# Performance work log

Hardware: AMD Instinct MI355X
Metric: run time of the kernel (lower is better)

## Reference

```python
import jax, jax.numpy as jnp
import numpy as np
import math

V, BS, D, L, H = 50257, 1024, 768, 12, 4
DH = D // H  # 192
B, T = 4, 1024


def setup_inputs() -> dict:
    key = jax.random.key(0)
    ks = jax.random.split(key, 18)
    s = 0.02
    inp = {
        "x": jax.random.randint(ks[0], (B, T), 0, V),
        "tok_emb": jax.random.normal(ks[1], (V, D), jnp.float32) * s,
        "pos_emb": jax.random.normal(ks[2], (BS, D), jnp.float32) * s,
        "ln1_s": jnp.ones((L, D), jnp.float32),
        "ln1_b": jnp.zeros((L, D), jnp.float32),
        "qkv_w": jax.random.normal(ks[3], (L, D, 3 * D), jnp.float32) * s,
        "qkv_b": jnp.zeros((L, 3 * D), jnp.float32),
        "ln2_s": jnp.ones((L, D), jnp.float32),
        "ln2_b": jnp.zeros((L, D), jnp.float32),
        "fc_w": jax.random.normal(ks[4], (L, D, 4 * D), jnp.float32) * s,
        "fc_b": jnp.zeros((L, 4 * D), jnp.float32),
        "proj_w": jax.random.normal(ks[5], (L, 4 * D, D), jnp.float32) * s,
        "proj_b": jnp.zeros((L, D), jnp.float32),
        "lnf_s": jnp.ones((D,), jnp.float32),
        "lnf_b": jnp.zeros((D,), jnp.float32),
        "head_w": jax.random.normal(ks[6], (D, V), jnp.float32) * s,
        "head_b": jnp.zeros((V,), jnp.float32),
    }
    return inp


def _ln(x, scale, shift):
    m = x.mean(-1, keepdims=True)
    v = jnp.mean((x - m) ** 2, axis=-1, keepdims=True)
    return (x - m) * jax.lax.rsqrt(v + 1e-5) * scale + shift


def _forward(x, tok_emb, pos_emb, ln1_s, ln1_b, qkv_w, qkv_b, ln2_s, ln2_b,
             fc_w, fc_b, proj_w, proj_b, lnf_s, lnf_b, head_w, head_b):
    Bx, Tx = x.shape
    h = tok_emb[x] + pos_emb[:Tx]  # [B,T,D]
    causal = jnp.tril(jnp.ones((Tx, Tx), bool))
    scale = 1.0 / math.sqrt(DH)

    def block(h, p):
        s1, b1, wq, bq, s2, b2, wf, bf, wp, bp = p
        # attention (no output projection, faithful to source)
        ln1 = _ln(h, s1, b1)
        qkv = ln1 @ wq + bq  # [B,T,3D]
        q, k, v = jnp.split(qkv, 3, axis=-1)
        q = q.reshape(Bx, Tx, H, DH)
        k = k.reshape(Bx, Tx, H, DH)
        v = v.reshape(Bx, Tx, H, DH)
        att = jnp.einsum('bthd,bshd->bhts', q, k) * scale
        att = jnp.where(causal, att, -jnp.inf)
        att = jax.nn.softmax(att, axis=-1)
        y = jnp.einsum('bhts,bshd->bthd', att, v).reshape(Bx, Tx, D)
        h = h + y
        # MLP (ReLU, despite attr named gelu in source)
        ln2 = _ln(h, s2, b2)
        m = jax.nn.relu(ln2 @ wf + bf) @ wp + bp
        return h + m, None

    h, _ = jax.lax.scan(block, h,
                        (ln1_s, ln1_b, qkv_w, qkv_b, ln2_s, ln2_b,
                         fc_w, fc_b, proj_w, proj_b))
    h = _ln(h, lnf_s, lnf_b)
    return h @ head_w + head_b  # [B,T,V]


def reference(x, tok_emb, pos_emb, ln1_s, ln1_b, qkv_w, qkv_b, ln2_s, ln2_b,
              fc_w, fc_b, proj_w, proj_b, lnf_s, lnf_b, head_w, head_b):
    return _forward(x, tok_emb, pos_emb, ln1_s, ln1_b, qkv_w, qkv_b,
                    ln2_s, ln2_b, fc_w, fc_b, proj_w, proj_b,
                    lnf_s, lnf_b, head_w, head_b)
```

## Files before the change

kernel.cpp:

```cpp
#include <hip/hip_runtime.h>
#include <stdint.h>

#define D_MODEL 768
#define NHEAD 4
#define DHEAD 192
#define SEQ 1024
#define NLAYER 12
#define NTOK 4096
#define NVOCAB 50257

typedef __attribute__((ext_vector_type(4))) float f32x4;
typedef __attribute__((ext_vector_type(4))) int i32x4;
typedef __attribute__((ext_vector_type(4))) unsigned short u16x4;

__device__ __forceinline__ unsigned short f2bf(float f) {
  unsigned u = __builtin_bit_cast(unsigned, f);
  u += 0x7FFFu + ((u >> 16) & 1u);
  return (unsigned short)(u >> 16);
}

#define GLDS(src, dst)                                                   \
  __builtin_amdgcn_global_load_lds(                                      \
      (const __attribute__((address_space(1))) void*)(src),              \
      (__attribute__((address_space(3))) void*)(dst), 16, 0, 0)

#define FENCE asm volatile("" ::: "memory")
#define BAR()                         \
  do {                                \
    FENCE;                            \
    __builtin_amdgcn_s_barrier();     \
    FENCE;                            \
  } while (0)

__global__ __launch_bounds__(256) void embed_kernel(
    const int* __restrict__ x, const float* __restrict__ tok,
    const float* __restrict__ pos, float* __restrict__ h) {
  int row = blockIdx.x;
  int t = row & (SEQ - 1);
  int id = x[row];
  const float* tp = tok + (long)id * D_MODEL;
  const float* pp = pos + (long)t * D_MODEL;
  float* hp = h + (long)row * D_MODEL;
  for (int j = threadIdx.x; j < D_MODEL; j += 256)
    hp[j] = tp[j] + pp[j];
}

__global__ __launch_bounds__(256) void ln_kernel(
    const float* __restrict__ h, const float* __restrict__ sc,
    const float* __restrict__ sh, unsigned short* __restrict__ out) {
  __shared__ float red[4];
  int row = blockIdx.x;
  const float* x = h + (long)row * D_MODEL;
  int tid = threadIdx.x;
  float v0 = x[tid], v1 = x[tid + 256], v2 = x[tid + 512];
  float s = v0 + v1 + v2;
  for (int o = 32; o > 0; o >>= 1) s += __shfl_xor(s, o);
  if ((tid & 63) == 0) red[tid >> 6] = s;
  __syncthreads();
  float mean = (red[0] + red[1] + red[2] + red[3]) * (1.0f / D_MODEL);
  __syncthreads();
  float d0 = v0 - mean, d1 = v1 - mean, d2 = v2 - mean;
  float q = d0 * d0 + d1 * d1 + d2 * d2;
  for (int o = 32; o > 0; o >>= 1) q += __shfl_xor(q, o);
  if ((tid & 63) == 0) red[tid >> 6] = q;
  __syncthreads();
  float var = (red[0] + red[1] + red[2] + red[3]) * (1.0f / D_MODEL);
  float r = rsqrtf(var + 1e-5f);
  unsigned short* op = out + (long)row * D_MODEL;
  op[tid]       = f2bf(d0 * r * sc[tid]       + sh[tid]);
  op[tid + 256] = f2bf(d1 * r * sc[tid + 256] + sh[tid + 256]);
  op[tid + 512] = f2bf(d2 * r * sc[tid + 512] + sh[tid + 512]);
}

__global__ __launch_bounds__(256) void wtrans3_kernel(
    const float* __restrict__ qw, const float* __restrict__ fw,
    const float* __restrict__ pw, unsigned short* __restrict__ tq,
    unsigned short* __restrict__ tf, unsigned short* __restrict__ tp) {
  __shared__ unsigned short tile[32][33];
  int bid = blockIdx.x;
  const float* src; unsigned short* dst; int K, N, nb;
  if (bid < 1728)               { src = qw; dst = tq; K = 768;  N = 2304; nb = 72; }
  else if ((bid -= 1728) < 2304){ src = fw; dst = tf; K = 768;  N = 3072; nb = 96; }
  else { bid -= 2304;             src = pw; dst = tp; K = 3072; N = 768;  nb = 24; }
  int n0 = (bid % nb) * 32, k0 = (bid / nb) * 32;
  int tx = threadIdx.x & 31, ty = threadIdx.x >> 5;
  #pragma unroll
  for (int i = 0; i < 4; ++i) {
    int k = k0 + ty + i * 8;
    tile[ty + i * 8][tx] = f2bf(src[(long)k * N + n0 + tx]);
  }
  __syncthreads();
  #pragma unroll
  for (int i = 0; i < 4; ++i) {
    int nn = n0 + ty + i * 8;
    dst[(long)nn * K + k0 + tx] = tile[tx][ty + i * 8];
  }
}

__global__ __launch_bounds__(256) void wtrans_kernel(
    const float* __restrict__ w, unsigned short* __restrict__ wt, int K, int N) {
  __shared__ unsigned short tile[32][33];
  int n0 = blockIdx.x * 32, k0 = blockIdx.y * 32;
  int tx = threadIdx.x, ty = threadIdx.y;
  int n = n0 + tx; if (n >= N) n = N - 1;
  #pragma unroll
  for (int i = 0; i < 4; ++i) {
    int k = k0 + ty + i * 8;
    tile[ty + i * 8][tx] = f2bf(w[(long)k * N + n]);
  }
  __syncthreads();
  #pragma unroll
  for (int i = 0; i < 4; ++i) {
    int nn = n0 + ty + i * 8;
    if (nn < N) wt[(long)nn * K + k0 + tx] = tile[tx][ty + i * 8];
  }
}

__global__ __launch_bounds__(256) void vt_kernel(
    const unsigned short* __restrict__ qkv, unsigned short* __restrict__ vt) {
  __shared__ unsigned short tile[32][33];
  int bh = blockIdx.z, b = bh >> 2, hh = bh & 3;
  int t0 = blockIdx.x * 32, f0 = blockIdx.y * 32;
  int tx = threadIdx.x, ty = threadIdx.y;
  const unsigned short* src = qkv + (long)b * SEQ * 2304 + 2 * D_MODEL + hh * DHEAD;
  #pragma unroll
  for (int i = 0; i < 4; ++i) {
    int t = t0 + ty + i * 8;
    tile[ty + i * 8][tx] = src[(long)t * 2304 + f0 + tx];
  }
  __syncthreads();
  unsigned short* dst = vt + (long)bh * DHEAD * SEQ;
  #pragma unroll
  for (int i = 0; i < 4; ++i) {
    int f = f0 + ty + i * 8;
    dst[(long)f * SEQ + t0 + tx] = tile[tx][ty + i * 8];
  }
}

__global__ __launch_bounds__(256) void fattn2_kernel(
    const unsigned short* __restrict__ qkv,
    const unsigned short* __restrict__ vt,
    float* __restrict__ h) {
  __shared__ float slds[16][1024];
  __shared__ unsigned short plds[16][1024];
  const float rscale = 0.07216878364870323f;
  int tid = threadIdx.x;
  int lane = tid & 63, wid = tid >> 6;
  int l15 = lane & 15, g = lane >> 4;
  int bid = blockIdx.x;
  int bh = bid & 15;
  int p = bid >> 4;
  int qt = (p < 32) ? (63 - p) : (p - 32);
  int b = bh >> 2, hh = bh & 3;
  const unsigned short* Qb = qkv + ((long)b * 1024 + qt * 16) * 2304 + hh * 192;
  const unsigned short* Kb = qkv + (long)b * 1024 * 2304 + 768 + hh * 192;
  const unsigned short* Vb = vt + (long)bh * 192 * 1024;
  int smax = qt * 16 + 16;
  int smax32 = (smax + 31) & ~31;

  i32x4 qfr[6];
  #pragma unroll
  for (int kb = 0; kb < 6; ++kb)
    qfr[kb] = *(const i32x4*)(Qb + (long)l15 * 2304 + kb * 32 + g * 8);
  int nsf = smax >> 4;
  int sfw = (nsf + 3) >> 2;
  int sf0 = wid * sfw;
  int sf1 = min(sf0 + sfw, nsf);
  for (int sf = sf0; sf < sf1; ++sf) {
    f32x4 sacc = {};
    #pragma unroll
    for (int kb = 0; kb < 6; ++kb) {
      i32x4 kf = *(const i32x4*)(Kb + (long)(sf * 16 + l15) * 2304 + kb * 32 + g * 8);
      asm("v_mfma_f32_16x16x32_bf16 %0, %1, %2, %0"
          : "+v"(sacc) : "v"(kf), "v"(qfr[kb]));
    }
    asm volatile("s_nop 7\n\ts_nop 7\n\ts_nop 7" : "+v"(sacc));
    f32x4 st;
    #pragma unroll
    for (int e = 0; e < 4; ++e) st[e] = sacc[e] * rscale;
    *(f32x4*)&slds[l15][sf * 16 + 4 * g] = st;
  }
  __syncthreads();

  {
    int q = tid >> 4, lane16 = tid & 15;
    int qg = qt * 16 + q;
    float mx = -3.0e38f;
    for (int s = lane16 * 4; s < smax32; s += 64) {
      f32x4 v = *(const f32x4*)&slds[q][s];
      #pragma unroll
      for (int e = 0; e < 4; ++e)
        if (s + e <= qg) mx = fmaxf(mx, v[e]);
    }
    #pragma unroll
    for (int o = 1; o < 16; o <<= 1) mx = fmaxf(mx, __shfl_xor(mx, o));
    float sum = 0.f;
    for (int s = lane16 * 4; s < smax32; s += 64) {
      f32x4 v = *(const f32x4*)&slds[q][s];
      #pragma unroll
      for (int e = 0; e < 4; ++e)
        v[e] = (s + e <= qg) ? __expf(v[e] - mx) : 0.f;
      *(f32x4*)&slds[q][s] = v;
      sum += v[0] + v[1] + v[2] + v[3];
    }
    #pragma unroll
    for (int o = 1; o < 16; o <<= 1) sum += __shfl_xor(sum, o);
    float inv = 1.0f / sum;
    for (int s = lane16 * 4; s < smax32; s += 64) {
      f32x4 v = *(const f32x4*)&slds[q][s];
      u16x4 o;
      #pragma unroll
      for (int e = 0; e < 4; ++e) o[e] = f2bf(v[e] * inv);
      *(u16x4*)&plds[q][s] = o;
    }
  }
  __syncthreads();

  f32x4 acc[3] = {};
  for (int ss = 0; ss < smax32; ss += 32) {
    i32x4 pf = *(const i32x4*)&plds[l15][ss + g * 8];
    #pragma unroll
    for (int nf = 0; nf < 3; ++nf) {
      i32x4 vf = *(const i32x4*)(Vb + (long)(wid * 48 + nf * 16 + l15) * 1024 + ss + g * 8);
      asm("v_mfma_f32_16x16x32_bf16 %0, %1, %2, %0"
          : "+v"(acc[nf]) : "v"(vf), "v"(pf));
    }
  }
  asm volatile("s_nop 7\n\ts_nop 7\n\ts_nop 7"
               : "+v"(acc[0]), "+v"(acc[1]), "+v"(acc[2]));
  float* hp = h + ((long)b * 1024 + qt * 16 + l15) * 768 + hh * 192 + wid * 48;
  #pragma unroll
  for (int nf = 0; nf < 3; ++nf) {
    float* cp = hp + nf * 16 + 4 * g;
    f32x4 old = *(f32x4*)cp;
    #pragma unroll
    for (int e = 0; e < 4; ++e) old[e] += acc[nf][e];
    *(f32x4*)cp = old;
  }
}

template<int MODE>
__global__ __launch_bounds__(512, 2) void gemm256_kernel(
    const unsigned short* __restrict__ A,
    const unsigned short* __restrict__ B,
    const float* __restrict__ bias,
    void* __restrict__ Cv, int ldc,
    int M, int N, int K, int mb) {
  __shared__ __align__(16) unsigned short lds[2][2][2][128 * 64];

  int tid = threadIdx.x;
  int lane = tid & 63;
  int wid = tid >> 6;
  int wm = wid >> 2;
  int wn = wid & 3;

  int bid = blockIdx.x;
  int mpx = mb >> 3;
  int xcd = bid & 7;
  int c = bid >> 3;
  int m0 = (xcd * mpx + (c & (mpx - 1))) * 256;
  int n0 = (c / mpx) * 256;

  auto stageA = [&](int buf, int half, int kt) {
    const unsigned short* src = A + (long)(m0 + half * 128) * K + kt * 64;
    #pragma unroll
    for (int i = 0; i < 2; ++i) {
      int chunk = i * 8 + wid;
      int r = chunk * 8 + (lane >> 3);
      int cc = ((lane & 7) ^ (lane >> 3)) << 3;
      GLDS(src + (long)r * K + cc, &lds[buf][0][half][chunk * 512]);
    }
  };
  auto stageB = [&](int buf, int half, int kt) {
    #pragma unroll
    for (int i = 0; i < 2; ++i) {
      int chunk = i * 8 + wid;
      int r = chunk * 8 + (lane >> 3);
      int cc = ((lane & 7) ^ (lane >> 3)) << 3;
      int rg = n0 + half * 128 + r;
      if (rg >= N) rg = N - 1;
      GLDS(B + (long)rg * K + kt * 64 + cc, &lds[buf][1][half][chunk * 512]);
    }
  };

  auto lda_frag = [&](int buf, int f, int s) -> i32x4 {
    int r = wm * 64 + (f & 3) * 16 + (lane & 15);
    int kb = s * 64 + ((lane >> 4) << 4);
    int off = r * 128 + (kb ^ ((r & 7) << 4));
    return *(const i32x4*)((const char*)&lds[buf][0][f >> 2][0] + off);
  };
  auto ldb_frag = [&](int buf, int gg, int s) -> i32x4 {
    int r = wn * 32 + (gg & 1) * 16 + (lane & 15);
    int kb = s * 64 + ((lane >> 4) << 4);
    int off = r * 128 + (kb ^ ((r & 7) << 4));
    return *(const i32x4*)((const char*)&lds[buf][1][gg >> 1][0] + off);
  };

  f32x4 acc[8][4] = {};
  i32x4 a[4][2], b[4][2];

  int nt = K / 64;

  stageA(0, 0, 0); stageB(0, 0, 0); stageB(0, 1, 0); stageA(0, 1, 0);
  stageA(1, 0, 1); stageB(1, 0, 1); stageB(1, 1, 1);
  asm volatile("s_waitcnt vmcnt(6)" ::: "memory");
  BAR();

  for (int t = 0; t < nt; ++t) {
    int buf = t & 1, nbuf = buf ^ 1;
    #pragma unroll
    for (int fi = 0; fi < 4; ++fi) {
      a[fi][0] = lda_frag(buf, fi, 0);
      a[fi][1] = lda_frag(buf, fi, 1);
    }
    #pragma unroll
    for (int gi = 0; gi < 2; ++gi) {
      b[gi][0] = ldb_frag(buf, gi, 0);
      b[gi][1] = ldb_frag(buf, gi, 1);
    }
    if (t + 1 < nt) stageA(nbuf, 1, t + 1);
    BAR();
    __builtin_amdgcn_s_setprio(1);
    #pragma unroll
    for (int s = 0; s < 2; ++s)
      #pragma unroll
      for (int fi = 0; fi < 4; ++fi)
        #pragma unroll
        for (int gi = 0; gi < 2; ++gi)
          asm("v_mfma_f32_16x16x32_bf16 %0, %1, %2, %0"
              : "+v"(acc[fi][gi]) : "v"(b[gi][s]), "v"(a[fi][s]));
    __builtin_amdgcn_s_setprio(0);
    BAR();
    #pragma unroll
    for (int gi = 2; gi < 4; ++gi) {
      b[gi][0] = ldb_frag(buf, gi, 0);
      b[gi][1] = ldb_frag(buf, gi, 1);
    }
    if (t + 2 < nt) stageA(buf, 0, t + 2);
    BAR();
    __builtin_amdgcn_s_setprio(1);
    #pragma unroll
    for (int s = 0; s < 2; ++s)
      #pragma unroll
      for (int fi = 0; fi < 4; ++fi)
        #pragma unroll
        for (int gi = 2; gi < 4; ++gi)
          asm("v_mfma_f32_16x16x32_bf16 %0, %1, %2, %0"
              : "+v"(acc[fi][gi]) : "v"(b[gi][s]), "v"(a[fi][s]));
    __builtin_amdgcn_s_setprio(0);
    BAR();
    #pragma unroll
    for (int fi = 0; fi < 4; ++fi) {
      a[fi][0] = lda_frag(buf, 4 + fi, 0);
      a[fi][1] = lda_frag(buf, 4 + fi, 1);
    }
    if (t + 2 < nt) stageB(buf, 0, t + 2);
    BAR();
    __builtin_amdgcn_s_setprio(1);
    #pragma unroll
    for (int s = 0; s < 2; ++s)
      #pragma unroll
      for (int fi = 0; fi < 4; ++fi)
        #pragma unroll
        for (int gi = 2; gi < 4; ++gi)
          asm("v_mfma_f32_16x16x32_bf16 %0, %1, %2, %0"
              : "+v"(acc[4 + fi][gi]) : "v"(b[gi][s]), "v"(a[fi][s]));
    __builtin_amdgcn_s_setprio(0);
    BAR();
    if (t + 2 < nt) {
      stageB(buf, 1, t + 2);
      asm volatile("s_waitcnt vmcnt(6)" ::: "memory");
    } else if (t + 1 < nt) {
      asm volatile("s_waitcnt vmcnt(0)" ::: "memory");
    }
    BAR();
    __builtin_amdgcn_s_setprio(1);
    #pragma unroll
    for (int s = 0; s < 2; ++s)
      #pragma unroll
      for (int fi = 0; fi < 4; ++fi)
        #pragma unroll
        for (int gi = 0; gi < 2; ++gi)
          asm("v_mfma_f32_16x16x32_bf16 %0, %1, %2, %0"
              : "+v"(acc[4 + fi][gi]) : "v"(b[gi][s]), "v"(a[fi][s]));
    __builtin_amdgcn_s_setprio(0);
    BAR();
  }

  int cr = lane & 15;
  int cg = (lane >> 4) << 2;
  #pragma unroll
  for (int f = 0; f < 8; ++f) {
    long row = m0 + wm * 64 + (f & 3) * 16 + (f >> 2) * 128 + cr;
    #pragma unroll
    for (int gg = 0; gg < 4; ++gg) {
      int col = n0 + wn * 32 + (gg & 1) * 16 + (gg >> 1) * 128 + cg;
      f32x4 v = acc[f][gg];
      if (MODE == 0 || MODE == 1) {
        f32x4 bv = *(const f32x4*)(bias + col);
        u16x4 o;
        #pragma unroll
        for (int r = 0; r < 4; ++r) {
          float tt = v[r] + bv[r];
          if (MODE == 1) tt = fmaxf(tt, 0.f);
          o[r] = f2bf(tt);
        }
        *(u16x4*)((unsigned short*)Cv + row * (long)ldc + col) = o;
      } else {
        float* cp = (float*)Cv + row * (long)ldc + col;
        if (col + 4 <= N) {
          f32x4 bv = *(const f32x4*)(bias + col);
          f32x4 o;
          #pragma unroll
          for (int r = 0; r < 4; ++r) o[r] = v[r] + bv[r];
          *(f32x4*)cp = o;
        } else {
          #pragma unroll
          for (int r = 0; r < 4; ++r)
            if (col + r < N) cp[r] = v[r] + bias[col + r];
        }
      }
    }
  }
}

#define BM 128
#define BN 128
#define BKK 32

template<int MODE>
__global__ __launch_bounds__(256) void gemm_kernel(
    const unsigned short* __restrict__ A, int lda,
    const unsigned short* __restrict__ B, int ldb,
    const float* __restrict__ bias,
    void* __restrict__ Cv, int ldc,
    int M, int N, int K,
    int NI, long sAo, long sAi, long sBo, long sBi,
    long sCo, long sCi, float alpha, int causal, int mblocks) {
  __shared__ __align__(16) unsigned short As[2][BM * BKK];
  __shared__ __align__(16) unsigned short Bs[2][BN * BKK];
  int z = blockIdx.z;
  int zo = z / NI, zi = z - zo * NI;
  A += zo * sAo + zi * sAi;
  B += zo * sBo + zi * sBi;
  long coff = zo * sCo + zi * sCi;

  int m0, n0;
  if (mblocks > 0) {
    int bid = blockIdx.x;
    int mpx = mblocks >> 3;
    int xcd = bid & 7;
    int c = bid >> 3;
    m0 = (xcd * mpx + (c & (mpx - 1))) * BM;
    n0 = (c / mpx) * BN;
  } else {
    m0 = blockIdx.y * BM;
    n0 = blockIdx.x * BN;
  }
  if (causal == 1 && n0 > m0 + BM - 1) return;
  int kmax = (causal == 2) ? min(K, m0 + BM) : K;

  int tid = threadIdx.x;
  int lane = tid & 63;
  int wave = tid >> 6;
  int wm = (wave >> 1) * 64;
  int wn = (wave & 1) * 64;

  auto stage = [&](int buf, int k0) {
    #pragma unroll
    for (int i = 0; i < 2; ++i) {
      int c0 = i * 256 + wave * 64;
      int cc = c0 + lane;
      int row = cc >> 2;
      int ko = (cc & 3) << 3;
      GLDS(A + (long)(m0 + row) * lda + k0 + ko, As[buf] + c0 * 8);
      int rg = n0 + row; if (rg >= N) rg = N - 1;
      GLDS(B + (long)rg * ldb + k0 + ko, Bs[buf] + c0 * 8);
    }
  };

  f32x4 acc[4][4] = {};
  int nt = kmax / BKK;
  stage(0, 0);
  __syncthreads();
  int cur = 0;
  for (int t = 0; t < nt; ++t) {
    if (t + 1 < nt) stage(cur ^ 1, (t + 1) * BKK);
    int lr = lane & 15;
    int kg = (lane >> 4) << 3;
    i32x4 af[4], bf[4];
    #pragma unroll
    for (int mi = 0; mi < 4; ++mi)
      af[mi] = *(const i32x4*)(As[cur] + (wm + mi * 16 + lr) * BKK + kg);
    #pragma unroll
    for (int ni = 0; ni < 4; ++ni)
      bf[ni] = *(const i32x4*)(Bs[cur] + (wn + ni * 16 + lr) * BKK + kg);
    #pragma unroll
    for (int mi = 0; mi < 4; ++mi)
      #pragma unroll
      for (int ni = 0; ni < 4; ++ni)
        asm("v_mfma_f32_16x16x32_bf16 %0, %1, %2, %0"
            : "+v"(acc[mi][ni]) : "v"(bf[ni]), "v"(af[mi]));
    __syncthreads();
    cur ^= 1;
  }

  int cm = lane & 15;
  int cg = (lane >> 4) << 2;
  #pragma unroll
  for (int mi = 0; mi < 4; ++mi) {
    long row = m0 + wm + mi * 16 + cm;
    #pragma unroll
    for (int ni = 0; ni < 4; ++ni) {
      int col = n0 + wn + ni * 16 + cg;
      f32x4 v = acc[mi][ni];
      if (MODE == 2) {
        #pragma unroll
        for (int r = 0; r < 4; ++r) v[r] *= alpha;
        *(f32x4*)((float*)Cv + coff + row * (long)ldc + col) = v;
      } else if (MODE == 0 || MODE == 1) {
        f32x4 bv = *(const f32x4*)(bias + col);
        u16x4 o;
        #pragma unroll
        for (int r = 0; r < 4; ++r) {
          float t = v[r] + bv[r];
          if (MODE == 1) t = fmaxf(t, 0.f);
          o[r] = f2bf(t);
        }
        *(u16x4*)((unsigned short*)Cv + coff + row * (long)ldc + col) = o;
      } else {
        float* cp = (float*)Cv + coff + row * (long)ldc + col;
        if (col + 4 <= N) {
          f32x4 bv = bias ? *(const f32x4*)(bias + col)
                          : f32x4{0.f, 0.f, 0.f, 0.f};
          if (MODE == 3) {
            f32x4 old = *(f32x4*)cp;
            #pragma unroll
            for (int r = 0; r < 4; ++r) old[r] += v[r] + bv[r];
            *(f32x4*)cp = old;
          } else {
            f32x4 o;
            #pragma unroll
            for (int r = 0; r < 4; ++r) o[r] = v[r] + bv[r];
            *(f32x4*)cp = o;
          }
        } else {
          #pragma unroll
          for (int r = 0; r < 4; ++r) {
            if (col + r < N) {
              float bvr = bias ? bias[col + r] : 0.f;
              if (MODE == 3) cp[r] += v[r] + bvr;
              else           cp[r] = v[r] + bvr;
            }
          }
        }
      }
    }
  }
}

extern "C" void kernel_launch(void* const* d_in, const int* in_sizes, int n_in,
                              void* d_out, int out_size, void* d_ws, size_t ws_size,
                              hipStream_t stream) {
  const int*   x       = (const int*)  d_in[0];
  const float* tok_emb = (const float*)d_in[1];
  const float* pos_emb = (const float*)d_in[2];
  const float* ln1_s   = (const float*)d_in[3];
  const float* ln1_b   = (const float*)d_in[4];
  const float* qkv_w   = (const float*)d_in[5];
  const float* qkv_b   = (const float*)d_in[6];
  const float* ln2_s   = (const float*)d_in[7];
  const float* ln2_b   = (const float*)d_in[8];
  const float* fc_w    = (const float*)d_in[9];
  const float* fc_b    = (const float*)d_in[10];
  const float* proj_w  = (const float*)d_in[11];
  const float* proj_b  = (const float*)d_in[12];
  const float* lnf_s   = (const float*)d_in[13];
  const float* lnf_b   = (const float*)d_in[14];
  const float* head_w  = (const float*)d_in[15];
  const float* head_b  = (const float*)d_in[16];

  char* ws = (char*)d_ws;
  size_t off = 0;
  auto alloc = [&](size_t bytes) {
    char* p = ws + off;
    off += (bytes + 255) & ~(size_t)255;
    return p;
  };
  float*          h   = (float*)         alloc((size_t)NTOK * D_MODEL * 4);
  unsigned short* lnb = (unsigned short*)alloc((size_t)NTOK * D_MODEL * 2);
  unsigned short* qkv = (unsigned short*)alloc((size_t)NTOK * 2304 * 2);
  unsigned short* vt  = (unsigned short*)alloc((size_t)16 * DHEAD * SEQ * 2);
  unsigned short* mid = (unsigned short*)alloc((size_t)NTOK * 3072 * 2);
  unsigned short* wtq = (unsigned short*)alloc((size_t)2304 * 768 * 2);
  unsigned short* wtf = (unsigned short*)alloc((size_t)3072 * 768 * 2);
  unsigned short* wtp = (unsigned short*)alloc((size_t)768 * 3072 * 2);
  unsigned short* wth = (unsigned short*)alloc((size_t)50304 * 768 * 2);

  embed_kernel<<<NTOK, 256, 0, stream>>>(x, tok_emb, pos_emb, h);

  for (int l = 0; l < NLAYER; ++l) {
    wtrans3_kernel<<<6336, 256, 0, stream>>>(
        qkv_w + (long)l * 768 * 2304, fc_w + (long)l * 768 * 3072,
        proj_w + (long)l * 3072 * 768, wtq, wtf, wtp);
    ln_kernel<<<NTOK, 256, 0, stream>>>(h, ln1_s + l * 768, ln1_b + l * 768, lnb);
    gemm256_kernel<0><<<16 * 9, 512, 0, stream>>>(
        lnb, wtq, qkv_b + l * 2304, qkv, 2304, 4096, 2304, 768, 16);
    vt_kernel<<<dim3(32, 6, 16), dim3(32, 8), 0, stream>>>(qkv, vt);
    fattn2_kernel<<<1024, 256, 0, stream>>>(qkv, vt, h);
    ln_kernel<<<NTOK, 256, 0, stream>>>(h, ln2_s + l * 768, ln2_b + l * 768, lnb);
    gemm256_kernel<1><<<16 * 12, 512, 0, stream>>>(
        lnb, wtf, fc_b + l * 3072, mid, 3072, 4096, 3072, 768, 16);
    gemm_kernel<3><<<192, 256, 0, stream>>>(
        mid, 3072, wtp, 3072, proj_b + l * 768, h, 768,
        4096, 768, 3072, 1, 0, 0, 0, 0, 0, 0, 1.0f, 0, 32);
  }

  wtrans_kernel<<<dim3(1571, 24), dim3(32, 8), 0, stream>>>(head_w, wth, 768, 50257);
  ln_kernel<<<NTOK, 256, 0, stream>>>(h, lnf_s, lnf_b, lnb);
  gemm256_kernel<4><<<16 * 197, 512, 0, stream>>>(
      lnb, wth, head_b, (float*)d_out, 50257, 4096, 50257, 768, 16);
}
```

Measured before the change: 3.258 ms.

## Replace three-phase attention with per-wave online-softmax flash attention

Rewrites the attention kernel so each wave owns a 16-query tile and streams 32-key blocks, using an online softmax (running max and sum with rescaling) instead of materialising the full score row in LDS. The old 48KB LDS buffers for fp32 scores and bf16 probabilities are replaced by a small per-wave staging buffer, and the block-wide barriers are removed. Query tiles are paired long/short across waves to balance causal work, and the grid shrinks from 1024 to 256 blocks. The cost is 48 accumulator registers per lane, a per-step rescale of all 12 accumulators, fewer blocks in flight, and K/V fragments re-read from global memory by each wave.

```diff
diff --git a/kernel.cpp b/kernel.cpp
--- a/kernel.cpp
+++ b/kernel.cpp
@@ -137,104 +137,114 @@
   }
 }
 
-__global__ __launch_bounds__(256) void fattn2_kernel(
+__global__ __launch_bounds__(256) void fattn3_kernel(
     const unsigned short* __restrict__ qkv,
     const unsigned short* __restrict__ vt,
     float* __restrict__ h) {
-  __shared__ float slds[16][1024];
-  __shared__ unsigned short plds[16][1024];
+  __shared__ __align__(16) unsigned plds[4][16][20];
   const float rscale = 0.07216878364870323f;
   int tid = threadIdx.x;
   int lane = tid & 63, wid = tid >> 6;
   int l15 = lane & 15, g = lane >> 4;
   int bid = blockIdx.x;
   int bh = bid & 15;
-  int p = bid >> 4;
-  int qt = (p < 32) ? (63 - p) : (p - 32);
+  int cc = bid >> 4;
+  int tau = cc * 4 + wid;
+  int qt = (tau & 1) ? (tau >> 1) : (63 - (tau >> 1));
   int b = bh >> 2, hh = bh & 3;
   const unsigned short* Qb = qkv + ((long)b * 1024 + qt * 16) * 2304 + hh * 192;
   const unsigned short* Kb = qkv + (long)b * 1024 * 2304 + 768 + hh * 192;
   const unsigned short* Vb = vt + (long)bh * 192 * 1024;
-  int smax = qt * 16 + 16;
-  int smax32 = (smax + 31) & ~31;
 
   i32x4 qfr[6];
   #pragma unroll
   for (int kb = 0; kb < 6; ++kb)
     qfr[kb] = *(const i32x4*)(Qb + (long)l15 * 2304 + kb * 32 + g * 8);
-  int nsf = smax >> 4;
-  int sfw = (nsf + 3) >> 2;
-  int sf0 = wid * sfw;
-  int sf1 = min(sf0 + sfw, nsf);
-  for (int sf = sf0; sf < sf1; ++sf) {
-    f32x4 sacc = {};
+
+  f32x4 Oa[12] = {};
+  float mrun = -3.0e38f, lrun = 0.f;
+  int qmy = qt * 16 + l15;
+  int nst = (qt + 2) >> 1;
+
+  for (int st = 0; st < nst; ++st) {
+    int s0 = st * 32;
+    f32x4 sacc[2] = {};
     #pragma unroll
     for (int kb = 0; kb < 6; ++kb) {
-      i32x4 kf = *(const i32x4*)(Kb + (long)(sf * 16 + l15) * 2304 + kb * 32 + g * 8);
+      i32x4 kf0 = *(const i32x4*)(Kb + (long)(s0 + l15) * 2304 + kb * 32 + g * 8);
+      i32x4 kf1 = *(const i32x4*)(Kb + (long)(s0 + 16 + l15) * 2304 + kb * 32 + g * 8);
       asm("v_mfma_f32_16x16x32_bf16 %0, %1, %2, %0"
-          : "+v"(sacc) : "v"(kf), "v"(qfr[kb]));
-    }
-    asm volatile("s_nop 7\n\ts_nop 7\n\ts_nop 7" : "+v"(sacc));
-    f32x4 st;
-    #pragma unroll
-    for (int e = 0; e < 4; ++e) st[e] = sacc[e] * rscale;
-    *(f32x4*)&slds[l15][sf * 16 + 4 * g] = st;
-  }
-  __syncthreads();
-
-  {
-    int q = tid >> 4, lane16 = tid & 15;
-    int qg = qt * 16 + q;
-    float mx = -3.0e38f;
-    for (int s = lane16 * 4; s < smax32; s += 64) {
-      f32x4 v = *(const f32x4*)&slds[q][s];
+          : "+v"(sacc[0]) : "v"(kf0), "v"(qfr[kb]));
+      asm("v_mfma_f32_16x16x32_bf16 %0, %1, %2, %0"
+          : "+v"(sacc[1]) : "v"(kf1), "v"(qfr[kb]));
+    }
+    asm volatile("s_nop 7\n\ts_nop 7\n\ts_nop 7" : "+v"(sacc[0]), "+v"(sacc[1]));
+    float v[2][4];
+    float tmax = -3.0e38f;
+    #pragma unroll
+    for (int sf = 0; sf < 2; ++sf)
+      #pragma unroll
+      for (int e = 0; e < 4; ++e) {
+        int s = s0 + sf * 16 + 4 * g + e;
+        float x = sacc[sf][e] * rscale;
+        x = (s <= qmy) ? x : -3.0e38f;
+        v[sf][e] = x;
+        tmax = fmaxf(tmax, x);
+      }
+    tmax = fmaxf(tmax, __shfl_xor(tmax, 16));
+    tmax = fmaxf(tmax, __shfl_xor(tmax, 32));
+    float mnew = fmaxf(mrun, tmax);
+    float corr = __expf(mrun - mnew);
+    mrun = mnew;
+    float ps = 0.f;
+    unsigned pk[4];
+    #pragma unroll
+    for (int sf = 0; sf < 2; ++sf) {
+      float e0 = __expf(v[sf][0] - mnew);
+      float e1 = __expf(v[sf][1] - mnew);
+      float e2 = __expf(v[sf][2] - mnew);
+      float e3 = __expf(v[sf][3] - mnew);
+      ps += (e0 + e1) + (e2 + e3);
+      pk[2 * sf]     = ((unsigned)f2bf(e1) << 16) | f2bf(e0);
+      pk[2 * sf + 1] = ((unsigned)f2bf(e3) << 16) | f2bf(e2);
+    }
+    ps += __shfl_xor(ps, 16);
+    ps += __shfl_xor(ps, 32);
+    lrun = lrun * corr + ps;
+    #pragma unroll
+    for (int df = 0; df < 12; ++df)
       #pragma unroll
       for (int e = 0; e < 4; ++e)
-        if (s + e <= qg) mx = fmaxf(mx, v[e]);
-    }
-    #pragma unroll
-    for (int o = 1; o < 16; o <<= 1) mx = fmaxf(mx, __shfl_xor(mx, o));
-    float sum = 0.f;
-    for (int s = lane16 * 4; s < smax32; s += 64) {
-      f32x4 v = *(const f32x4*)&slds[q][s];
-      #pragma unroll
-      for (int e = 0; e < 4; ++e)
-        v[e] = (s + e <= qg) ? __expf(v[e] - mx) : 0.f;
-      *(f32x4*)&slds[q][s] = v;
-      sum += v[0] + v[1] + v[2] + v[3];
-    }
-    #pragma unroll
-    for (int o = 1; o < 16; o <<= 1) sum += __shfl_xor(sum, o);
-    float inv = 1.0f / sum;
-    for (int s = lane16 * 4; s < smax32; s += 64) {
-      f32x4 v = *(const f32x4*)&slds[q][s];
-      u16x4 o;
-      #pragma unroll
-      for (int e = 0; e < 4; ++e) o[e] = f2bf(v[e] * inv);
-      *(u16x4*)&plds[q][s] = o;
-    }
-  }
-  __syncthreads();
-
-  f32x4 acc[3] = {};
-  for (int ss = 0; ss < smax32; ss += 32) {
-    i32x4 pf = *(const i32x4*)&plds[l15][ss + g * 8];
-    #pragma unroll
-    for (int nf = 0; nf < 3; ++nf) {
-      i32x4 vf = *(const i32x4*)(Vb + (long)(wid * 48 + nf * 16 + l15) * 1024 + ss + g * 8);
+        Oa[df][e] *= corr;
+    plds[wid][l15][2 * g]         = pk[0];
+    plds[wid][l15][2 * g + 1]     = pk[1];
+    plds[wid][l15][8 + 2 * g]     = pk[2];
+    plds[wid][l15][8 + 2 * g + 1] = pk[3];
+    asm volatile("s_waitcnt lgkmcnt(0)" ::: "memory");
+    __builtin_amdgcn_sched_barrier(0);
+    i32x4 pf = *(const i32x4*)&plds[wid][l15][4 * g];
+    __builtin_amdgcn_sched_barrier(0);
+    #pragma unroll
+    for (int df = 0; df < 12; ++df) {
+      i32x4 vf = *(const i32x4*)(Vb + (long)(df * 16 + l15) * 1024 + s0 + g * 8);
       asm("v_mfma_f32_16x16x32_bf16 %0, %1, %2, %0"
-          : "+v"(acc[nf]) : "v"(vf), "v"(pf));
-    }
-  }
-  asm volatile("s_nop 7\n\ts_nop 7\n\ts_nop 7"
-               : "+v"(acc[0]), "+v"(acc[1]), "+v"(acc[2]));
-  float* hp = h + ((long)b * 1024 + qt * 16 + l15) * 768 + hh * 192 + wid * 48;
-  #pragma unroll
-  for (int nf = 0; nf < 3; ++nf) {
-    float* cp = hp + nf * 16 + 4 * g;
+          : "+v"(Oa[df]) : "v"(vf), "v"(pf));
+    }
+    asm volatile("s_nop 7\n\ts_nop 7\n\ts_nop 7"
+                 : "+v"(Oa[0]), "+v"(Oa[1]), "+v"(Oa[2]), "+v"(Oa[3]),
+                   "+v"(Oa[4]), "+v"(Oa[5]), "+v"(Oa[6]), "+v"(Oa[7]),
+                   "+v"(Oa[8]), "+v"(Oa[9]), "+v"(Oa[10]), "+v"(Oa[11]));
+    __builtin_amdgcn_sched_barrier(0);
+  }
+
+  float inv = 1.0f / lrun;
+  float* hp = h + ((long)b * 1024 + qt * 16 + l15) * 768 + hh * 192;
+  #pragma unroll
+  for (int df = 0; df < 12; ++df) {
+    float* cp = hp + df * 16 + 4 * g;
     f32x4 old = *(f32x4*)cp;
     #pragma unroll
-    for (int e = 0; e < 4; ++e) old[e] += acc[nf][e];
+    for (int e = 0; e < 4; ++e) old[e] += Oa[df][e] * inv;
     *(f32x4*)cp = old;
   }
 }
@@ -607,7 +617,7 @@
     gemm256_kernel<0><<<16 * 9, 512, 0, stream>>>(
         lnb, wtq, qkv_b + l * 2304, qkv, 2304, 4096, 2304, 768, 16);
     vt_kernel<<<dim3(32, 6, 16), dim3(32, 8), 0, stream>>>(qkv, vt);
-    fattn2_kernel<<<1024, 256, 0, stream>>>(qkv, vt, h);
+    fattn3_kernel<<<256, 256, 0, stream>>>(qkv, vt, h);
     ln_kernel<<<NTOK, 256, 0, stream>>>(h, ln2_s + l * 768, ln2_b + l * 768, lnb);
     gemm256_kernel<1><<<16 * 12, 512, 0, stream>>>(
         lnb, wtf, fc_b + l * 3072, mid, 3072, 4096, 3072, 768, 16);
```

Result: slower. 4.227 ms (+29.7%).
